# Optimization experiments

Hardware: AMD Instinct MI355X
Metric: run time of the kernel (lower is better)

Reference implementation:

```python
import jax, jax.numpy as jnp
import numpy as np

E = 640000   # number of scattered rows (edges)
N = 50000    # number of segments / attention keys
V = 128      # values_dim
K = 128      # keys_dim


def setup_inputs() -> dict:
    key = jax.random.key(0)
    k1, k2, k3, k4, k5 = jax.random.split(key, 5)
    scattered_values = jax.random.normal(k1, (E, V), dtype=jnp.float32)
    indices = jax.random.randint(k2, (E,), 0, N)
    attn_keys = jax.random.normal(k3, (N, K), dtype=jnp.float32)
    # nn.Linear(keys_dim, values_dim): weight [V, K], bias [V]
    lim = 1.0 / np.sqrt(K)
    W = jax.random.uniform(k4, (V, K), minval=-lim, maxval=lim, dtype=jnp.float32)
    b = jax.random.uniform(k5, (V,), minval=-lim, maxval=lim, dtype=jnp.float32)
    return {"scattered_values": scattered_values, "indices": indices,
            "attn_keys": attn_keys, "W": W, "b": b}


def reference(scattered_values, indices, attn_keys, W, b):
    # Project keys: [N, K] @ [K, V] + [V] -> [N, V]
    keys_proj = jnp.einsum('nk,vk->nv', attn_keys, W) + b
    # Gather projected key for each scattered row: [E, V]
    gathered = keys_proj[indices]
    # Per-row attention logit: [E]
    probs = jnp.sum(scattered_values * gathered, axis=1)
    # Segment (scatter) softmax over rows sharing the same index
    seg_max = jax.ops.segment_max(probs, indices, num_segments=N)
    ex = jnp.exp(probs - seg_max[indices])
    denom = jax.ops.segment_sum(ex, indices, num_segments=N)
    scores = ex / denom[indices]                      # [E]
    # Weighted segment-sum aggregation: [N, V]
    attn_applied = jax.ops.segment_sum(scattered_values * scores[:, None],
                                       indices, num_segments=N)
    return scores, attn_applied
```

## Files before the change

kernel.cpp:

```cpp
#include <hip/hip_runtime.h>
#include <cstdint>

#define DIM 128
#define CAP 64

__global__ __launch_bounds__(256) void hist_kernel(const int* __restrict__ idx,
                                                   int* __restrict__ count,
                                                   int* __restrict__ bucket,
                                                   int E) {
  int e = blockIdx.x * 256 + threadIdx.x;
  if (e >= E) return;
  int n = idx[e];
  int r = atomicAdd(&count[n], 1);
  if (r < CAP) bucket[n * CAP + r] = e;
}

__global__ __launch_bounds__(256) void keys_proj_gemm(const float* __restrict__ A,
                                                      const float* __restrict__ W,
                                                      const float* __restrict__ bias,
                                                      float* __restrict__ C,
                                                      int Nrows) {
  __shared__ float As[16][128];
  __shared__ float Ws[16][128];
  int t = threadIdx.x;
  int tx = t & 15;
  int ty = t >> 4;
  int n0 = blockIdx.x * 128;

  float acc[8][8];
#pragma unroll
  for (int r = 0; r < 8; ++r)
#pragma unroll
    for (int c = 0; c < 8; ++c) acc[r][c] = 0.f;

  for (int k0 = 0; k0 < DIM; k0 += 16) {
#pragma unroll
    for (int i = 0; i < 2; ++i) {
      int f = t + i * 256;
      int n = f >> 2;
      int kq = f & 3;
      int gn = n0 + n;
      if (gn >= Nrows) gn = Nrows - 1;
      const float4 a4 = *(const float4*)(A + (size_t)gn * DIM + k0 + kq * 4);
      As[kq * 4 + 0][n] = a4.x; As[kq * 4 + 1][n] = a4.y;
      As[kq * 4 + 2][n] = a4.z; As[kq * 4 + 3][n] = a4.w;
      const float4 w4 = *(const float4*)(W + (size_t)n * DIM + k0 + kq * 4);
      Ws[kq * 4 + 0][n] = w4.x; Ws[kq * 4 + 1][n] = w4.y;
      Ws[kq * 4 + 2][n] = w4.z; Ws[kq * 4 + 3][n] = w4.w;
    }
    __syncthreads();
#pragma unroll
    for (int kk = 0; kk < 16; ++kk) {
      float av[8], wv[8];
      *(float4*)&av[0] = *(const float4*)&As[kk][ty * 8];
      *(float4*)&av[4] = *(const float4*)&As[kk][ty * 8 + 4];
      *(float4*)&wv[0] = *(const float4*)&Ws[kk][tx * 8];
      *(float4*)&wv[4] = *(const float4*)&Ws[kk][tx * 8 + 4];
#pragma unroll
      for (int r = 0; r < 8; ++r)
#pragma unroll
        for (int c = 0; c < 8; ++c)
          acc[r][c] = fmaf(av[r], wv[c], acc[r][c]);
    }
    __syncthreads();
  }

#pragma unroll
  for (int r = 0; r < 8; ++r) {
    int gn = n0 + ty * 8 + r;
    if (gn < Nrows) {
#pragma unroll
      for (int c = 0; c < 8; c += 4) {
        int v = tx * 8 + c;
        float4 o;
        o.x = acc[r][c + 0] + bias[v + 0];
        o.y = acc[r][c + 1] + bias[v + 1];
        o.z = acc[r][c + 2] + bias[v + 2];
        o.w = acc[r][c + 3] + bias[v + 3];
        *(float4*)(C + (size_t)gn * DIM + v) = o;
      }
    }
  }
}

__global__ __launch_bounds__(256) void seg_attn_kernel(const float* __restrict__ sv,
                                                       const int* __restrict__ count,
                                                       const int* __restrict__ bucket,
                                                       const float* __restrict__ kp,
                                                       float* __restrict__ scores,
                                                       float* __restrict__ attn,
                                                       int Nseg) {
  int gw = (blockIdx.x * 256 + threadIdx.x) >> 6;
  int lane = threadIdx.x & 63;
  if (gw >= Nseg) return;
  int n = gw;
  int cnt = count[n];
  cnt = cnt > CAP ? CAP : cnt;
  int g = lane >> 4;
  int q = lane & 15;

  const float4* kprow = (const float4*)(kp + (size_t)n * DIM);
  float4 kpa = kprow[q * 2 + 0];
  float4 kpb = kprow[q * 2 + 1];

  int e_lane = (lane < cnt) ? bucket[n * CAP + lane] : 0;

  int iters = (cnt + 3) >> 2;
  float psave = 0.f;
  for (int j = 0; j < iters; ++j) {
    int ei = 4 * j + g;
    int e = __shfl(e_lane, ei);
    const float4* src = (const float4*)(sv + (size_t)e * DIM) + q * 2;
    float4 a0 = src[0];
    float4 a1 = src[1];
    float d = a0.x * kpa.x + a0.y * kpa.y + a0.z * kpa.z + a0.w * kpa.w
            + a1.x * kpb.x + a1.y * kpb.y + a1.z * kpb.z + a1.w * kpb.w;
    d += __shfl_xor(d, 1);
    d += __shfl_xor(d, 2);
    d += __shfl_xor(d, 4);
    d += __shfl_xor(d, 8);
    if (q == j) psave = d;
  }
  float p_lane = __shfl(psave, (lane & 3) * 16 + (lane >> 2));
  if (lane >= cnt) p_lane = -3.4e38f;

  float m = p_lane;
#pragma unroll
  for (int d = 1; d < 64; d <<= 1) m = fmaxf(m, __shfl_xor(m, d));
  float ex = (lane < cnt) ? __expf(p_lane - m) : 0.f;
  float denom = ex;
#pragma unroll
  for (int d = 1; d < 64; d <<= 1) denom += __shfl_xor(denom, d);
  float sc = ex / denom;
  if (lane < cnt) scores[e_lane] = sc;

  float4 acc0 = {0.f, 0.f, 0.f, 0.f};
  float4 acc1 = {0.f, 0.f, 0.f, 0.f};
  for (int j = 0; j < iters; ++j) {
    int ei = 4 * j + g;
    int e = __shfl(e_lane, ei);
    float s = __shfl(sc, ei);
    const float4* src = (const float4*)(sv + (size_t)e * DIM) + q * 2;
    float4 a0 = src[0];
    float4 a1 = src[1];
    acc0.x = fmaf(s, a0.x, acc0.x); acc0.y = fmaf(s, a0.y, acc0.y);
    acc0.z = fmaf(s, a0.z, acc0.z); acc0.w = fmaf(s, a0.w, acc0.w);
    acc1.x = fmaf(s, a1.x, acc1.x); acc1.y = fmaf(s, a1.y, acc1.y);
    acc1.z = fmaf(s, a1.z, acc1.z); acc1.w = fmaf(s, a1.w, acc1.w);
  }
  float* accf = (float*)&acc0;
#pragma unroll
  for (int mask = 16; mask < 64; mask <<= 1) {
    acc0.x += __shfl_xor(acc0.x, mask); acc0.y += __shfl_xor(acc0.y, mask);
    acc0.z += __shfl_xor(acc0.z, mask); acc0.w += __shfl_xor(acc0.w, mask);
    acc1.x += __shfl_xor(acc1.x, mask); acc1.y += __shfl_xor(acc1.y, mask);
    acc1.z += __shfl_xor(acc1.z, mask); acc1.w += __shfl_xor(acc1.w, mask);
  }
  (void)accf;
  if (g == 0) {
    float4* dst = (float4*)(attn + (size_t)n * DIM) + q * 2;
    dst[0] = acc0;
    dst[1] = acc1;
  }
}

extern "C" void kernel_launch(void* const* d_in, const int* in_sizes, int n_in,
                              void* d_out, int out_size, void* d_ws, size_t ws_size,
                              hipStream_t stream) {
  const float* sv   = (const float*)d_in[0];
  const int*   idx  = (const int*)d_in[1];
  const float* A    = (const float*)d_in[2];
  const float* W    = (const float*)d_in[3];
  const float* bias = (const float*)d_in[4];

  const int E = in_sizes[1];
  const int N = in_sizes[2] / DIM;

  float* scores = (float*)d_out;
  float* attn   = (float*)d_out + E;

  char* ws = (char*)d_ws;
  size_t off_bucket = ((size_t)N * 4 + 255) & ~(size_t)255;
  size_t off_kp     = off_bucket + (size_t)N * CAP * 4;
  int*   count  = (int*)ws;
  int*   bucket = (int*)(ws + off_bucket);
  float* kp     = (float*)(ws + off_kp);

  hipMemsetAsync(count, 0, (size_t)N * 4, stream);

  hist_kernel<<<(E + 255) / 256, 256, 0, stream>>>(idx, count, bucket, E);
  keys_proj_gemm<<<(N + 127) / 128, 256, 0, stream>>>(A, W, bias, kp, N);
  seg_attn_kernel<<<(N + 3) / 4, 256, 0, stream>>>(sv, count, bucket, kp,
                                                   scores, attn, N);
}
```

Baseline: 545.9 us.

## Fuse segment softmax and aggregation with online softmax in one pass

Replaces the two passes over each segment's scattered rows (a logit pass, then a weighted-sum pass that reloads the rows) with a single online-softmax pass. Each lane group keeps a running max, denominator and rescaled output, and the groups are merged across the wave at the end. This is meant to halve the global reads of scattered_values, which dominate the kernel's memory traffic. In exchange it adds extra exp and rescale arithmetic per iteration, and its numerics differ slightly from the two-pass version.

```diff
diff --git a/kernel.cpp b/kernel.cpp
--- a/kernel.cpp
+++ b/kernel.cpp
@@ -107,8 +107,14 @@
 
   int iters = (cnt + 3) >> 2;
   float psave = 0.f;
+  float m_g = -3.4e38f;
+  float l_g = 0.f;
+  float4 O0 = {0.f, 0.f, 0.f, 0.f};
+  float4 O1 = {0.f, 0.f, 0.f, 0.f};
+
   for (int j = 0; j < iters; ++j) {
     int ei = 4 * j + g;
+    bool valid = ei < cnt;
     int e = __shfl(e_lane, ei);
     const float4* src = (const float4*)(sv + (size_t)e * DIM) + q * 2;
     float4 a0 = src[0];
@@ -119,48 +125,49 @@
     d += __shfl_xor(d, 2);
     d += __shfl_xor(d, 4);
     d += __shfl_xor(d, 8);
+    if (!valid) d = -3.4e38f;
     if (q == j) psave = d;
-  }
+
+    float mn = fmaxf(m_g, d);
+    float factor = __expf(m_g - mn);
+    float w = valid ? __expf(d - mn) : 0.f;
+    l_g = fmaf(l_g, factor, w);
+    O0.x = fmaf(O0.x, factor, w * a0.x); O0.y = fmaf(O0.y, factor, w * a0.y);
+    O0.z = fmaf(O0.z, factor, w * a0.z); O0.w = fmaf(O0.w, factor, w * a0.w);
+    O1.x = fmaf(O1.x, factor, w * a1.x); O1.y = fmaf(O1.y, factor, w * a1.y);
+    O1.z = fmaf(O1.z, factor, w * a1.z); O1.w = fmaf(O1.w, factor, w * a1.w);
+    m_g = mn;
+  }
+
+  float M = m_g;
+  M = fmaxf(M, __shfl_xor(M, 16));
+  M = fmaxf(M, __shfl_xor(M, 32));
+  float scale = __expf(m_g - M);
+
+  float denom = l_g * scale;
+  denom += __shfl_xor(denom, 16);
+  denom += __shfl_xor(denom, 32);
+  float rinv = denom > 0.f ? __frcp_rn(denom) : 0.f;
+
   float p_lane = __shfl(psave, (lane & 3) * 16 + (lane >> 2));
-  if (lane >= cnt) p_lane = -3.4e38f;
-
-  float m = p_lane;
-#pragma unroll
-  for (int d = 1; d < 64; d <<= 1) m = fmaxf(m, __shfl_xor(m, d));
-  float ex = (lane < cnt) ? __expf(p_lane - m) : 0.f;
-  float denom = ex;
-#pragma unroll
-  for (int d = 1; d < 64; d <<= 1) denom += __shfl_xor(denom, d);
-  float sc = ex / denom;
-  if (lane < cnt) scores[e_lane] = sc;
-
-  float4 acc0 = {0.f, 0.f, 0.f, 0.f};
-  float4 acc1 = {0.f, 0.f, 0.f, 0.f};
-  for (int j = 0; j < iters; ++j) {
-    int ei = 4 * j + g;
-    int e = __shfl(e_lane, ei);
-    float s = __shfl(sc, ei);
-    const float4* src = (const float4*)(sv + (size_t)e * DIM) + q * 2;
-    float4 a0 = src[0];
-    float4 a1 = src[1];
-    acc0.x = fmaf(s, a0.x, acc0.x); acc0.y = fmaf(s, a0.y, acc0.y);
-    acc0.z = fmaf(s, a0.z, acc0.z); acc0.w = fmaf(s, a0.w, acc0.w);
-    acc1.x = fmaf(s, a1.x, acc1.x); acc1.y = fmaf(s, a1.y, acc1.y);
-    acc1.z = fmaf(s, a1.z, acc1.z); acc1.w = fmaf(s, a1.w, acc1.w);
-  }
-  float* accf = (float*)&acc0;
+  if (lane < cnt) scores[e_lane] = __expf(p_lane - M) * rinv;
+
+  O0.x *= scale; O0.y *= scale; O0.z *= scale; O0.w *= scale;
+  O1.x *= scale; O1.y *= scale; O1.z *= scale; O1.w *= scale;
 #pragma unroll
   for (int mask = 16; mask < 64; mask <<= 1) {
-    acc0.x += __shfl_xor(acc0.x, mask); acc0.y += __shfl_xor(acc0.y, mask);
-    acc0.z += __shfl_xor(acc0.z, mask); acc0.w += __shfl_xor(acc0.w, mask);
-    acc1.x += __shfl_xor(acc1.x, mask); acc1.y += __shfl_xor(acc1.y, mask);
-    acc1.z += __shfl_xor(acc1.z, mask); acc1.w += __shfl_xor(acc1.w, mask);
-  }
-  (void)accf;
+    O0.x += __shfl_xor(O0.x, mask); O0.y += __shfl_xor(O0.y, mask);
+    O0.z += __shfl_xor(O0.z, mask); O0.w += __shfl_xor(O0.w, mask);
+    O1.x += __shfl_xor(O1.x, mask); O1.y += __shfl_xor(O1.y, mask);
+    O1.z += __shfl_xor(O1.z, mask); O1.w += __shfl_xor(O1.w, mask);
+  }
   if (g == 0) {
+    float4 o0 = O0, o1 = O1;
+    o0.x *= rinv; o0.y *= rinv; o0.z *= rinv; o0.w *= rinv;
+    o1.x *= rinv; o1.y *= rinv; o1.z *= rinv; o1.w *= rinv;
     float4* dst = (float4*)(attn + (size_t)n * DIM) + q * 2;
-    dst[0] = acc0;
-    dst[1] = acc1;
+    dst[0] = o0;
+    dst[1] = o1;
   }
 }
 
```

Result: no change. 541.5 us (-0.8%).
